# Performance work log

Measured on AMD Instinct MI355X. Metric: run time of the kernel, lower is better.

## Reference

```python
import jax, jax.numpy as jnp
import numpy as np

T, N, E = 10, 10000, 320000
IN_C, HID_C, OUT_C = 128, 128, 64
K = 3


def _edge_weights(src, dst, n):
    # PyG ChebConv norm with sym normalization, lambda_max=2:
    # L_hat = -D^{-1/2} A D^{-1/2} (self loops removed, diagonal 0)
    valid = (src != dst).astype(jnp.float32)  # remove_self_loops
    deg = jax.ops.segment_sum(valid, src, num_segments=n)
    dinv = jnp.where(deg > 0, jax.lax.rsqrt(jnp.maximum(deg, 1.0)), 0.0)
    return -valid * dinv[src] * dinv[dst]  # [E]


def _agg(w, src, dst, x, n):
    # (L_hat @ x): messages from src to dst
    return jax.ops.segment_sum(w[:, None] * x[src], dst, num_segments=n)


def _cheb(x, W, b, w, src, dst, n):
    # ChebConv K=3: T0=x, T1=L_hat x, T2=2 L_hat T1 - T0
    Tx0 = x
    Tx1 = _agg(w, src, dst, Tx0, n)
    Tx2 = 2.0 * _agg(w, src, dst, Tx1, n) - Tx0
    return Tx0 @ W[0] + Tx1 @ W[1] + Tx2 @ W[2] + b


def setup_inputs() -> dict:
    key = jax.random.key(0)
    ks = jax.random.split(key, 20)
    features_seq = jax.random.normal(ks[0], (T, N, IN_C), dtype=jnp.float32)
    edges_seq = jax.random.randint(ks[1], (T, 2, E), 0, N, dtype=jnp.int64)
    s = 0.05
    inp = {"features_seq": features_seq, "edges_seq": edges_seq}
    names = ["Wxz", "Whz", "Wxr", "Whr", "Wxh", "Whh"]
    ins = [IN_C, HID_C, IN_C, HID_C, IN_C, HID_C]
    for i, (nm, ci) in enumerate(zip(names, ins)):
        inp[nm] = jax.random.normal(ks[2 + i], (K, ci, HID_C), dtype=jnp.float32) * s
        inp["b" + nm[1:].lower()] = jnp.zeros((HID_C,), dtype=jnp.float32)
    inp["Wp"] = jax.random.normal(ks[10], (HID_C, OUT_C), dtype=jnp.float32) * s
    inp["bp"] = jnp.zeros((OUT_C,), dtype=jnp.float32)
    return inp


def reference(features_seq, edges_seq, Wxz, bxz, Whz, bhz, Wxr, bxr, Whr, bhr,
              Wxh, bxh, Whh, bhh, Wp, bp):
    n = features_seq.shape[1]

    def step(h, xt_et):
        x, e = xt_et
        src, dst = e[0], e[1]
        w = _edge_weights(src, dst, n)
        z = jax.nn.sigmoid(_cheb(x, Wxz, bxz, w, src, dst, n)
                           + _cheb(h, Whz, bhz, w, src, dst, n))
        r = jax.nn.sigmoid(_cheb(x, Wxr, bxr, w, src, dst, n)
                           + _cheb(h, Whr, bhr, w, src, dst, n))
        h_tilde = jnp.tanh(_cheb(x, Wxh, bxh, w, src, dst, n)
                           + _cheb(h * r, Whh, bhh, w, src, dst, n))
        h_new = z * h + (1.0 - z) * h_tilde
        return h_new, None

    h0 = jnp.zeros((n, HID_C), dtype=features_seq.dtype)
    h, _ = jax.lax.scan(step, h0, (features_seq, edges_seq))
    return h @ Wp + bp
```

## Files before the change

### kernel.cpp

```cpp
#include <hip/hip_runtime.h>

#define T_STEPS 10
#define NN 10000
#define EE 320000
#define CC 128
#define NC (NN*CC)
#define BHIST 32
#define EPB (EE/BHIST)
#define NCHK 40

typedef unsigned short u16;
typedef unsigned int u32;
typedef __attribute__((ext_vector_type(8))) short bf16x8;
typedef __attribute__((ext_vector_type(4))) float f32x4;

__device__ __forceinline__ float sigmoidf_(float x){ return 1.f/(1.f+__expf(-x)); }
__device__ __forceinline__ float tanhf_(float x){
  x = fminf(15.f, fmaxf(-15.f, x));
  float e = __expf(2.f*x);
  return (e-1.f)/(e+1.f);
}
__device__ __forceinline__ u16 f2bf(float f){
  u32 u = __float_as_uint(f);
  u32 r = u + 0x7fffu + ((u>>16)&1u);
  return (u16)(r>>16);
}
__device__ __forceinline__ float bf2f(u16 s){
  return __uint_as_float(((u32)s)<<16);
}
__device__ __forceinline__ float blo(u32 u){ return __uint_as_float(u<<16); }
__device__ __forceinline__ float bhi(u32 u){ return __uint_as_float(u & 0xffff0000u); }
__device__ __forceinline__ void gload16(const void* g, void* l){
  __builtin_amdgcn_global_load_lds(
    (const __attribute__((address_space(1))) void*)g,
    (__attribute__((address_space(3))) void*)l, 16, 0, 0);
}

__global__ __launch_bounds__(256) void prep_kernel(
    const float* __restrict__ Wxz, const float* __restrict__ Whz,
    const float* __restrict__ Wxr, const float* __restrict__ Whr,
    const float* __restrict__ Wxh, const float* __restrict__ Whh,
    const float* __restrict__ bxz, const float* __restrict__ bhz,
    const float* __restrict__ bxr, const float* __restrict__ bhr,
    const float* __restrict__ bxh, const float* __restrict__ bhh,
    const float* __restrict__ Wp,
    u16* __restrict__ WbigT, u16* __restrict__ WrT, u16* __restrict__ WpT,
    float* __restrict__ bz, float* __restrict__ br, float* __restrict__ bht,
    u16* __restrict__ h)
{
  int idx = blockIdx.x*256 + threadIdx.x;
  if (idx < NC) h[idx] = 0;
  if (idx < 384*768) {
    int c = idx / 768, k = idx - c*768;
    int gate = c >> 7, cc = c & 127;
    int hside = (k >= 384);
    int kk = hside ? k - 384 : k;
    int blk = kk >> 7, row = kk & 127;
    const float* W = nullptr;
    if (!hside) W = (gate==0) ? Wxz : (gate==1) ? Wxr : Wxh;
    else if (gate==0) W = Whz; else if (gate==1) W = Whr;
    float v = 0.f;
    if (W) {
      int base = row*CC + cc;
      float w0 = W[base], w1 = W[CC*CC + base], w2 = W[2*CC*CC + base];
      v = (blk==0) ? (w0 - w2) : (blk==1) ? w1 : (2.f*w2);
    }
    WbigT[idx] = f2bf(v);
  }
  if (idx < 128*384) {
    int c = idx / 384, k = idx - c*384;
    int blk = k >> 7, row = k & 127;
    int base = row*CC + c;
    float w0 = Whh[base], w1 = Whh[CC*CC+base], w2 = Whh[2*CC*CC+base];
    WrT[idx] = f2bf((blk==0) ? (w0-w2) : (blk==1) ? w1 : (2.f*w2));
  }
  if (idx < 64*128) {
    int c = idx >> 7, k = idx & 127;
    WpT[idx] = f2bf(Wp[k*64 + c]);
  }
  if (idx < CC) {
    bz[idx]  = bxz[idx] + bhz[idx];
    br[idx]  = bxr[idx] + bhr[idx];
    bht[idx] = bxh[idx] + bhh[idx];
  }
}

__global__ __launch_bounds__(256) void xconv_kernel(const float* __restrict__ x, u16* __restrict__ xb, int n4){
  int i = blockIdx.x*256 + threadIdx.x;
  if (i >= n4) return;
  long long o = (long long)i*4;
  float4 v = *(const float4*)(x + o);
  u32 u0 = (u32)f2bf(v.x) | ((u32)f2bf(v.y)<<16);
  u32 u1 = (u32)f2bf(v.z) | ((u32)f2bf(v.w)<<16);
  uint2 r; r.x=u0; r.y=u1;
  *(uint2*)(xb + o) = r;
}

__global__ __launch_bounds__(512) void hist_kernel(const int* __restrict__ edges,
                                                   u32* __restrict__ histP){
  __shared__ u32 hist[NN];
  int t = blockIdx.y, b = blockIdx.x, tid = threadIdx.x;
  for (int i = tid; i < NN; i += 512) hist[i] = 0;
  __syncthreads();
  const int* src = edges + (size_t)t*2*EE;
  const int* dst = src + EE;
  int e1 = b*EPB + EPB;
  #pragma unroll 4
  for (int e = b*EPB + tid; e < e1; e += 512){
    int s = src[e], d = dst[e];
    if (s != d){
      atomicAdd(&hist[s], 1u);
      atomicAdd(&hist[d], 1u << 16);
    }
  }
  __syncthreads();
  u32* hp = histP + ((size_t)t*BHIST + b)*NN;
  for (int i = tid; i < NN; i += 512) hp[i] = hist[i];
}

__global__ __launch_bounds__(256) void reduce_scan_kernel(u32* __restrict__ histP,
                                                          int* __restrict__ rowptr_all,
                                                          int* __restrict__ chunk_tot,
                                                          float* __restrict__ dinv_all){
  int t = blockIdx.y, ch = blockIdx.x, tid = threadIdx.x;
  int d = ch*256 + tid;
  u32 run=0, degs=0;
  if (d < NN){
    size_t base = (size_t)t*BHIST*NN + d;
    #pragma unroll
    for (int b=0;b<BHIST;++b){
      size_t ix = base + (size_t)b*NN;
      u32 v = histP[ix];
      histP[ix] = (v & 0xffffu) | (run<<16);
      run += v>>16;
      degs += v & 0xffffu;
    }
    dinv_all[t*NN+d] = degs>0 ? rsqrtf((float)degs) : 0.f;
  }
  int lane = tid&63, wv = tid>>6;
  int s = (int)run;
  #pragma unroll
  for (int off=1; off<64; off<<=1){
    int u = __shfl_up(s, off, 64);
    if (lane>=off) s += u;
  }
  __shared__ int wsum[4];
  if (lane==63) wsum[wv] = s;
  __syncthreads();
  int add = 0;
  #pragma unroll
  for (int w=0; w<3; ++w) if (w < wv) add += wsum[w];
  int incl = s + add;
  if (d < NN) rowptr_all[(size_t)t*(NN+1)+d] = incl - (int)run;
  if (tid==255) chunk_tot[t*NCHK + ch] = incl;
}

__global__ __launch_bounds__(64) void scanb_kernel(const int* __restrict__ chunk_tot,
                                                   int* __restrict__ chunk_base,
                                                   int* __restrict__ rowptr_all){
  int t = blockIdx.x; int lane = threadIdx.x;
  int v = (lane < NCHK) ? chunk_tot[t*NCHK+lane] : 0;
  int s = v;
  #pragma unroll
  for (int off=1; off<64; off<<=1){
    int u = __shfl_up(s, off, 64);
    if (lane>=off) s += u;
  }
  if (lane < NCHK) chunk_base[t*NCHK+lane] = s - v;
  if (lane == NCHK-1) rowptr_all[(size_t)t*(NN+1)+NN] = s;
}

__global__ __launch_bounds__(256) void scanc_kernel(int* __restrict__ rowptr_all,
                                                    const int* __restrict__ chunk_base){
  int t = blockIdx.y, ch = blockIdx.x;
  int d = ch*256 + threadIdx.x;
  if (d < NN) rowptr_all[(size_t)t*(NN+1)+d] += chunk_base[t*NCHK+ch];
}

__global__ __launch_bounds__(512) void place_kernel(const int* __restrict__ edges,
                                                    const int* __restrict__ rowptr_all,
                                                    const u32* __restrict__ histP,
                                                    u16* __restrict__ colA_all){
  __shared__ int slot[NN];
  int t = blockIdx.y, b = blockIdx.x, tid = threadIdx.x;
  const int* rowptr = rowptr_all + (size_t)t*(NN+1);
  const u32* hp = histP + ((size_t)t*BHIST + b)*NN;
  for (int i = tid; i < NN; i += 512) slot[i] = rowptr[i] + (int)(hp[i] >> 16);
  __syncthreads();
  const int* src = edges + (size_t)t*2*EE;
  const int* dst = src + EE;
  u16* colA = colA_all + (size_t)t*EE;
  int e1 = b*EPB + EPB;
  #pragma unroll 4
  for (int e = b*EPB + tid; e < e1; e += 512){
    int s = src[e], d = dst[e];
    if (s != d){
      int pos = atomicAdd(&slot[d], 1);
      colA[pos] = (u16)s;
    }
  }
}

__device__ __forceinline__ void spmm_row4(const int* __restrict__ rowptr, const u16* __restrict__ colA,
                                          const float* __restrict__ dinv,
                                          const u16* __restrict__ in, u16* __restrict__ out,
                                          int wb, int wave, int lane){
  int row = wb*4 + wave;
  int k0 = rowptr[row], k1 = rowptr[row+1];
  int q = lane >> 4, cl = lane & 15;
  float a0=0.f,a1=0.f,a2=0.f,a3=0.f,a4=0.f,a5=0.f,a6=0.f,a7=0.f;
  #pragma unroll 2
  for (int k = k0 + q; k < k1; k += 4){
    int s = colA[k];
    float w = dinv[s];
    uint4 u = *(const uint4*)(in + (size_t)s*CC + cl*8);
    a0 = fmaf(w, blo(u.x), a0);  a1 = fmaf(w, bhi(u.x), a1);
    a2 = fmaf(w, blo(u.y), a2);  a3 = fmaf(w, bhi(u.y), a3);
    a4 = fmaf(w, blo(u.z), a4);  a5 = fmaf(w, bhi(u.z), a5);
    a6 = fmaf(w, blo(u.w), a6);  a7 = fmaf(w, bhi(u.w), a7);
  }
  a0 += __shfl_xor(a0,16); a1 += __shfl_xor(a1,16);
  a2 += __shfl_xor(a2,16); a3 += __shfl_xor(a3,16);
  a4 += __shfl_xor(a4,16); a5 += __shfl_xor(a5,16);
  a6 += __shfl_xor(a6,16); a7 += __shfl_xor(a7,16);
  a0 += __shfl_xor(a0,32); a1 += __shfl_xor(a1,32);
  a2 += __shfl_xor(a2,32); a3 += __shfl_xor(a3,32);
  a4 += __shfl_xor(a4,32); a5 += __shfl_xor(a5,32);
  a6 += __shfl_xor(a6,32); a7 += __shfl_xor(a7,32);
  if (q == 0){
    float wrow = -dinv[row];
    uint4 r;
    r.x = (u32)f2bf(wrow*a0) | ((u32)f2bf(wrow*a1)<<16);
    r.y = (u32)f2bf(wrow*a2) | ((u32)f2bf(wrow*a3)<<16);
    r.z = (u32)f2bf(wrow*a4) | ((u32)f2bf(wrow*a5)<<16);
    r.w = (u32)f2bf(wrow*a6) | ((u32)f2bf(wrow*a7)<<16);
    *(uint4*)(out + (size_t)row*CC + cl*8) = r;
  }
}

__global__ __launch_bounds__(256) void spmm_kernel(const int* __restrict__ rowptr, const u16* __restrict__ colA,
                                                   const float* __restrict__ dinv,
                                                   const u16* __restrict__ in, u16* __restrict__ out){
  int wave = threadIdx.x >> 6, lane = threadIdx.x & 63;
  int wb = blockIdx.x;
  if (wb >= NN/4) return;
  spmm_row4(rowptr, colA, dinv, in, out, wb, wave, lane);
}

__global__ __launch_bounds__(256) void spmm2_kernel(const int* __restrict__ rowptr, const u16* __restrict__ colA,
                                                    const float* __restrict__ dinv,
                                                    const u16* __restrict__ in0, u16* __restrict__ out0,
                                                    const u16* __restrict__ in1, u16* __restrict__ out1){
  int wave = threadIdx.x >> 6, lane = threadIdx.x & 63;
  int bid = blockIdx.x;
  int xcd = bid & 7;
  int inp = xcd >> 2;
  int wb  = (bid >> 3)*4 + (xcd & 3);
  if (wb >= NN/4) return;
  spmm_row4(rowptr, colA, dinv, inp?in1:in0, inp?out1:out0, wb, wave, lane);
}

template<int NSEG, int KDIM, int EPI, int SWZN>
__global__ __launch_bounds__(256) void mgemm_kernel(
    const u16* __restrict__ A0, const u16* __restrict__ A1, const u16* __restrict__ A2,
    const u16* __restrict__ A3, const u16* __restrict__ A4, const u16* __restrict__ A5,
    const u16* __restrict__ Bt,
    const float* __restrict__ bias0, const float* __restrict__ bias1,
    const u16* __restrict__ hbuf,
    float* __restrict__ zbuf, float* __restrict__ chx,
    u16* __restrict__ hr_out, u16* __restrict__ h_out,
    float* __restrict__ out_f)
{
  __shared__ __align__(16) u16 As[64*64];
  __shared__ __align__(16) u16 Bs[64*64];
  const u16* segs[6] = {A0,A1,A2,A3,A4,A5};
  int tid = threadIdx.x, lane = tid & 63, wvi = tid >> 6;
  int m0, n0;
  if (SWZN > 0){
    int bid = blockIdx.x;
    int j = bid >> 3;
    int mt = (bid & 7)*20 + (j % 20);
    if (mt >= 157) return;
    m0 = mt*64; n0 = (j/20)*64;
  } else {
    m0 = blockIdx.x*64; n0 = blockIdx.y*64;
  }
  int wr = wvi >> 1, wc = wvi & 1;

  f32x4 acc[2][2] = {};

  int c0 = wvi*64 + lane;
  int r0 = c0 >> 3, cc0 = c0 & 7;
  int scw = cc0 ^ (r0 & 7);
  int grow0 = m0 + r0;      if (grow0 > NN-1) grow0 = NN-1;
  int grow1 = m0 + r0 + 32; if (grow1 > NN-1) grow1 = NN-1;
  int nrow0 = n0 + r0, nrow1 = nrow0 + 32;
  u16* ldsA0 = (u16*)As + (size_t)wvi*64*8;
  u16* ldsA1 = ldsA0 + 256*8;
  u16* ldsB0 = (u16*)Bs + (size_t)wvi*64*8;
  u16* ldsB1 = ldsB0 + 256*8;

  int rl = lane & 15, rg = lane >> 4, sw = rl & 7;
  int rowa0 = wr*32 + rl, rowb0 = wc*32 + rl;
  int offA[2][2], offB[2][2];
  #pragma unroll
  for (int mf=0; mf<2; ++mf)
    #pragma unroll
    for (int ks=0; ks<2; ++ks){
      offA[mf][ks] = (rowa0 + mf*16)*128 + ((((ks<<2)+rg) ^ sw)<<4);
      offB[mf][ks] = (rowb0 + mf*16)*128 + ((((ks<<2)+rg) ^ sw)<<4);
    }

  const int ktend = (EPI==1 && n0 >= 256) ? NSEG : NSEG*2;
  for (int kt=0; kt<ktend; ++kt){
    const u16* __restrict__ Aseg = segs[kt>>1];
    int ko = (kt&1)*64;
    __syncthreads();
    gload16(Aseg + (size_t)grow0*CC + ko + scw*8, ldsA0);
    gload16(Aseg + (size_t)grow1*CC + ko + scw*8, ldsA1);
    gload16(Bt + (size_t)nrow0*KDIM + kt*64 + scw*8, ldsB0);
    gload16(Bt + (size_t)nrow1*KDIM + kt*64 + scw*8, ldsB1);
    __syncthreads();
    #pragma unroll
    for (int ks=0; ks<2; ++ks){
      bf16x8 a0 = *(const bf16x8*)((const char*)As + offA[0][ks]);
      bf16x8 a1 = *(const bf16x8*)((const char*)As + offA[1][ks]);
      bf16x8 b0 = *(const bf16x8*)((const char*)Bs + offB[0][ks]);
      bf16x8 b1 = *(const bf16x8*)((const char*)Bs + offB[1][ks]);
      acc[0][0] = __builtin_amdgcn_mfma_f32_16x16x32_bf16(a0, b0, acc[0][0], 0,0,0);
      acc[0][1] = __builtin_amdgcn_mfma_f32_16x16x32_bf16(a0, b1, acc[0][1], 0,0,0);
      acc[1][0] = __builtin_amdgcn_mfma_f32_16x16x32_bf16(a1, b0, acc[1][0], 0,0,0);
      acc[1][1] = __builtin_amdgcn_mfma_f32_16x16x32_bf16(a1, b1, acc[1][1], 0,0,0);
    }
  }

  #pragma unroll
  for (int mf=0; mf<2; ++mf){
    #pragma unroll
    for (int nf=0; nf<2; ++nf){
      #pragma unroll
      for (int r=0; r<4; ++r){
        int grow = m0 + wr*32 + mf*16 + rg*4 + r;
        if (grow >= NN) continue;
        int gcol = n0 + wc*32 + nf*16 + rl;
        float v = acc[mf][nf][r];
        if (EPI==0){
          out_f[(size_t)grow*64 + gcol] = v + bias0[gcol];
        } else if (EPI==1){
          int gate = gcol >> 7, c = gcol & 127;
          size_t idx = (size_t)grow*CC + c;
          if (gate==0)      zbuf[idx] = sigmoidf_(v + bias0[c]);
          else if (gate==1){
            float rr = sigmoidf_(v + bias1[c]);
            hr_out[idx] = f2bf(rr * bf2f(hbuf[idx]));
          } else            chx[idx] = v;
        } else {
          size_t idx = (size_t)grow*CC + gcol;
          float pre = v + chx[idx] + bias0[gcol];
          float ht = tanhf_(pre);
          float zz = zbuf[idx];
          float hv = bf2f(hbuf[idx]);
          h_out[idx] = f2bf(fmaf(zz, hv - ht, ht));
        }
      }
    }
  }
}

extern "C" void kernel_launch(void* const* d_in, const int* in_sizes, int n_in,
                              void* d_out, int out_size, void* d_ws, size_t ws_size,
                              hipStream_t stream)
{
  (void)in_sizes; (void)n_in; (void)out_size; (void)ws_size;
  const float* feat = (const float*)d_in[0];
  const int*   edges = (const int*)d_in[1];
  const float* Wxz=(const float*)d_in[2];  const float* bxz=(const float*)d_in[3];
  const float* Whz=(const float*)d_in[4];  const float* bhz=(const float*)d_in[5];
  const float* Wxr=(const float*)d_in[6];  const float* bxr=(const float*)d_in[7];
  const float* Whr=(const float*)d_in[8];  const float* bhr=(const float*)d_in[9];
  const float* Wxh=(const float*)d_in[10]; const float* bxh=(const float*)d_in[11];
  const float* Whh=(const float*)d_in[12]; const float* bhh=(const float*)d_in[13];
  const float* Wp =(const float*)d_in[14]; const float* bp =(const float*)d_in[15];
  float* out = (float*)d_out;

  char* p = (char*)d_ws;
  auto alloc = [&](size_t bytes)->char* {
    char* r = p; p += (bytes + 255) & ~(size_t)255; return r;
  };
  u16* xb   = (u16*)alloc((size_t)T_STEPS*NC*2);
  u16* h    = (u16*)alloc((size_t)NC*2);
  u16* a1x  = (u16*)alloc((size_t)NC*2);
  u16* a2x  = (u16*)alloc((size_t)NC*2);
  u16* a1h  = (u16*)alloc((size_t)NC*2);
  u16* a2h  = (u16*)alloc((size_t)NC*2);
  u16* hr   = (u16*)alloc((size_t)NC*2);
  float* zbuf = (float*)alloc((size_t)NC*4);
  float* chx  = (float*)alloc((size_t)NC*4);
  u16* WbigT = (u16*)alloc(384*768*2);
  u16* WrT   = (u16*)alloc(128*384*2);
  u16* WpT   = (u16*)alloc(64*128*2);
  float* bz  = (float*)alloc(CC*4);
  float* br  = (float*)alloc(CC*4);
  float* bht = (float*)alloc(CC*4);
  float* dinv_all = (float*)alloc((size_t)T_STEPS*NN*4);
  int* rowptr_all = (int*)alloc((size_t)T_STEPS*(NN+1)*4);
  u16* colA_all   = (u16*)alloc((size_t)T_STEPS*EE*2);
  int* chunk_tot  = (int*)alloc((size_t)T_STEPS*NCHK*4);
  int* chunk_base = (int*)alloc((size_t)T_STEPS*NCHK*4);
  u32* histP = (u32*)hr;

  prep_kernel<<<NC/256, 256, 0, stream>>>(Wxz,Whz,Wxr,Whr,Wxh,Whh,
                                          bxz,bhz,bxr,bhr,bxh,bhh, Wp,
                                          WbigT, WrT, WpT, bz, br, bht, h);
  xconv_kernel<<<(T_STEPS*NC/4 + 255)/256, 256, 0, stream>>>(feat, xb, T_STEPS*NC/4);

  hist_kernel<<<dim3(BHIST, T_STEPS), 512, 0, stream>>>(edges, histP);
  reduce_scan_kernel<<<dim3(NCHK, T_STEPS), 256, 0, stream>>>(histP, rowptr_all, chunk_tot, dinv_all);
  scanb_kernel<<<T_STEPS, 64, 0, stream>>>(chunk_tot, chunk_base, rowptr_all);
  scanc_kernel<<<dim3(NCHK, T_STEPS), 256, 0, stream>>>(rowptr_all, chunk_base);
  place_kernel<<<dim3(BHIST, T_STEPS), 512, 0, stream>>>(edges, rowptr_all, histP, colA_all);

  for (int t=0; t<T_STEPS; ++t){
    const int*   rowptr = rowptr_all + (size_t)t*(NN+1);
    const u16*   colA   = colA_all + (size_t)t*EE;
    const float* dinv   = dinv_all + (size_t)t*NN;
    const u16*   x      = xb + (size_t)t*NC;

    spmm2_kernel<<<dim3(2*(NN/4)), 256, 0, stream>>>(rowptr,colA,dinv, x,a1x, h,a1h);
    spmm2_kernel<<<dim3(2*(NN/4)), 256, 0, stream>>>(rowptr,colA,dinv, a1x,a2x, a1h,a2h);

    mgemm_kernel<6,768,1,6><<<dim3(8*20*6), 256, 0, stream>>>(
        x,a1x,a2x,h,a1h,a2h, WbigT, bz, br, h, zbuf, chx, hr, nullptr, nullptr);

    spmm_kernel<<<dim3(NN/4), 256, 0, stream>>>(rowptr,colA,dinv, hr, a1x);
    spmm_kernel<<<dim3(NN/4), 256, 0, stream>>>(rowptr,colA,dinv, a1x, a2x);

    mgemm_kernel<3,384,2,2><<<dim3(8*20*2), 256, 0, stream>>>(
        hr,a1x,a2x,nullptr,nullptr,nullptr, WrT, bht, nullptr, h, zbuf, chx,
        nullptr, h, nullptr);
  }

  mgemm_kernel<1,128,0,0><<<dim3(157,1), 256, 0, stream>>>(
      h,nullptr,nullptr,nullptr,nullptr,nullptr, WpT, bp, nullptr,
      nullptr, nullptr, nullptr, nullptr, nullptr, out);
}
```

Baseline: 879.1 us.

## Partition place kernel by row range and widen GEMM K-tile to 128

The CSR place kernel now splits each timestep's work into 8 destination-row ranges by 4 edge slices. Each block holds a smaller shared slot array and skips edges outside its row range, which cuts LDS use and may raise occupancy, at the cost of reading every edge 8 times. The MFMA GEMM now loads full 128-wide K tiles per segment with a 16-way XOR swizzle, halving the number of loop iterations and __syncthreads barriers. In exchange it doubles the LDS footprint per block. Correctness of the place kernel relies on the histogram prefix offsets for edge slice es being stored at hist block es*8, which holds because 4 slices map onto 32 hist blocks.

```diff
diff --git a/kernel.cpp b/kernel.cpp
--- a/kernel.cpp
+++ b/kernel.cpp
@@ -8,6 +8,10 @@
 #define BHIST 32
 #define EPB (EE/BHIST)
 #define NCHK 40
+#define PRS 8
+#define PES 4
+#define PROWS (NN/PRS)
+#define PEDG (EE/PES)
 
 typedef unsigned short u16;
 typedef unsigned int u32;
@@ -181,22 +185,28 @@
                                                     const int* __restrict__ rowptr_all,
                                                     const u32* __restrict__ histP,
                                                     u16* __restrict__ colA_all){
-  __shared__ int slot[NN];
+  __shared__ int slot[PROWS];
   int t = blockIdx.y, b = blockIdx.x, tid = threadIdx.x;
+  int rs = b >> 2, es = b & 3;
+  int lo = rs*PROWS, hi = lo + PROWS;
   const int* rowptr = rowptr_all + (size_t)t*(NN+1);
-  const u32* hp = histP + ((size_t)t*BHIST + b)*NN;
-  for (int i = tid; i < NN; i += 512) slot[i] = rowptr[i] + (int)(hp[i] >> 16);
+  const u32* hp = histP + ((size_t)t*BHIST + es*8)*NN;
+  for (int i = tid; i < PROWS; i += 512)
+    slot[i] = rowptr[lo+i] + (int)(hp[lo+i] >> 16);
   __syncthreads();
   const int* src = edges + (size_t)t*2*EE;
   const int* dst = src + EE;
   u16* colA = colA_all + (size_t)t*EE;
-  int e1 = b*EPB + EPB;
+  int e1 = es*PEDG + PEDG;
   #pragma unroll 4
-  for (int e = b*EPB + tid; e < e1; e += 512){
-    int s = src[e], d = dst[e];
-    if (s != d){
-      int pos = atomicAdd(&slot[d], 1);
-      colA[pos] = (u16)s;
+  for (int e = es*PEDG + tid; e < e1; e += 512){
+    int d = dst[e];
+    if (d >= lo && d < hi){
+      int s = src[e];
+      if (s != d){
+        int pos = atomicAdd(&slot[d-lo], 1);
+        colA[pos] = (u16)s;
+      }
     }
   }
 }
@@ -271,8 +281,8 @@
     u16* __restrict__ hr_out, u16* __restrict__ h_out,
     float* __restrict__ out_f)
 {
-  __shared__ __align__(16) u16 As[64*64];
-  __shared__ __align__(16) u16 Bs[64*64];
+  __shared__ __align__(16) u16 As[64*128];
+  __shared__ __align__(16) u16 Bs[64*128];
   const u16* segs[6] = {A0,A1,A2,A3,A4,A5};
   int tid = threadIdx.x, lane = tid & 63, wvi = tid >> 6;
   int m0, n0;
@@ -289,40 +299,35 @@
 
   f32x4 acc[2][2] = {};
 
-  int c0 = wvi*64 + lane;
-  int r0 = c0 >> 3, cc0 = c0 & 7;
-  int scw = cc0 ^ (r0 & 7);
-  int grow0 = m0 + r0;      if (grow0 > NN-1) grow0 = NN-1;
-  int grow1 = m0 + r0 + 32; if (grow1 > NN-1) grow1 = NN-1;
-  int nrow0 = n0 + r0, nrow1 = nrow0 + 32;
-  u16* ldsA0 = (u16*)As + (size_t)wvi*64*8;
-  u16* ldsA1 = ldsA0 + 256*8;
-  u16* ldsB0 = (u16*)Bs + (size_t)wvi*64*8;
-  u16* ldsB1 = ldsB0 + 256*8;
-
-  int rl = lane & 15, rg = lane >> 4, sw = rl & 7;
-  int rowa0 = wr*32 + rl, rowb0 = wc*32 + rl;
-  int offA[2][2], offB[2][2];
+  int c_lo = wvi*64 + lane;
+  int rl = lane & 15, rg = lane >> 4;
+  int offA[2][4], offB[2][4];
   #pragma unroll
   for (int mf=0; mf<2; ++mf)
     #pragma unroll
-    for (int ks=0; ks<2; ++ks){
-      offA[mf][ks] = (rowa0 + mf*16)*128 + ((((ks<<2)+rg) ^ sw)<<4);
-      offB[mf][ks] = (rowb0 + mf*16)*128 + ((((ks<<2)+rg) ^ sw)<<4);
-    }
-
-  const int ktend = (EPI==1 && n0 >= 256) ? NSEG : NSEG*2;
+    for (int ks=0; ks<4; ++ks){
+      offA[mf][ks] = (wr*32 + mf*16 + rl)*256 + ((((ks<<2)+rg) ^ rl)<<4);
+      offB[mf][ks] = (wc*32 + mf*16 + rl)*256 + ((((ks<<2)+rg) ^ rl)<<4);
+    }
+
+  const int ktend = (EPI==1 && n0 >= 256) ? (NSEG/2) : NSEG;
   for (int kt=0; kt<ktend; ++kt){
-    const u16* __restrict__ Aseg = segs[kt>>1];
-    int ko = (kt&1)*64;
-    __syncthreads();
-    gload16(Aseg + (size_t)grow0*CC + ko + scw*8, ldsA0);
-    gload16(Aseg + (size_t)grow1*CC + ko + scw*8, ldsA1);
-    gload16(Bt + (size_t)nrow0*KDIM + kt*64 + scw*8, ldsB0);
-    gload16(Bt + (size_t)nrow1*KDIM + kt*64 + scw*8, ldsB1);
+    const u16* __restrict__ Aseg = segs[kt];
     __syncthreads();
     #pragma unroll
-    for (int ks=0; ks<2; ++ks){
+    for (int i=0;i<4;++i){
+      int c = i*256 + c_lo;
+      int row = c >> 4, slot = c & 15;
+      int scw = slot ^ (row & 15);
+      int grow = m0 + row; if (grow > NN-1) grow = NN-1;
+      gload16(Aseg + (size_t)grow*CC + scw*8,
+              (u16*)As + ((size_t)i*256 + wvi*64)*8);
+      gload16(Bt + (size_t)(n0 + row)*KDIM + kt*128 + scw*8,
+              (u16*)Bs + ((size_t)i*256 + wvi*64)*8);
+    }
+    __syncthreads();
+    #pragma unroll
+    for (int ks=0; ks<4; ++ks){
       bf16x8 a0 = *(const bf16x8*)((const char*)As + offA[0][ks]);
       bf16x8 a1 = *(const bf16x8*)((const char*)As + offA[1][ks]);
       bf16x8 b0 = *(const bf16x8*)((const char*)Bs + offB[0][ks]);
@@ -418,7 +423,7 @@
   reduce_scan_kernel<<<dim3(NCHK, T_STEPS), 256, 0, stream>>>(histP, rowptr_all, chunk_tot, dinv_all);
   scanb_kernel<<<T_STEPS, 64, 0, stream>>>(chunk_tot, chunk_base, rowptr_all);
   scanc_kernel<<<dim3(NCHK, T_STEPS), 256, 0, stream>>>(rowptr_all, chunk_base);
-  place_kernel<<<dim3(BHIST, T_STEPS), 512, 0, stream>>>(edges, rowptr_all, histP, colA_all);
+  place_kernel<<<dim3(PRS*PES, T_STEPS), 512, 0, stream>>>(edges, rowptr_all, histP, colA_all);
 
   for (int t=0; t<T_STEPS; ++t){
     const int*   rowptr = rowptr_all + (size_t)t*(NN+1);
```

Measured after the change: 923.7 us. 1.05x slower.
